# Optimization experiments

Measured on AMD Instinct MI355X. Metric: run time of the kernel, lower is better.

Reference implementation:

```python
import jax, jax.numpy as jnp
import numpy as np

MARGIN = 0.3


def setup_inputs() -> dict:
    key = jax.random.key(0)
    k1, k2 = jax.random.split(key)
    embeddings = jax.random.normal(k1, (4096, 128), dtype=jnp.float32)
    labels = jax.random.randint(k2, (4096,), 0, 256, dtype=jnp.int64)
    return {"embeddings": embeddings, "labels": labels}


def reference(embeddings, labels):
    # L2-normalize rows (same as F.normalize(p=2, dim=1), eps=1e-12)
    norm = jnp.maximum(jnp.linalg.norm(embeddings, axis=1, keepdims=True), 1e-12)
    e = embeddings / norm
    # cosine distance matrix [N, N]
    dist = 1.0 - e @ e.T

    same = labels[None, :] == labels[:, None]          # [N, N]
    n = labels.shape[0]
    eye = jnp.eye(n, dtype=bool)
    pos_mask = same & ~eye                             # positives excl. self
    neg_mask = ~same

    # dist in [0, 2]; finite sentinels keep max/min well-defined per row
    hardest_pos = jnp.max(jnp.where(pos_mask, dist, -1.0), axis=1)
    hardest_neg = jnp.min(jnp.where(neg_mask, dist, 3.0), axis=1)

    valid = jnp.any(pos_mask, axis=1) & jnp.any(neg_mask, axis=1)
    per_row = jax.nn.relu(hardest_pos - hardest_neg + MARGIN)
    loss_sum = jnp.sum(jnp.where(valid, per_row, 0.0))
    count = jnp.sum(valid)
    return loss_sum / jnp.maximum(count, 1).astype(loss_sum.dtype)
```

## Files before the change

### kernel.cpp

```cpp
#include <hip/hip_runtime.h>
#include <stdint.h>

typedef __bf16 bf16x8 __attribute__((ext_vector_type(8)));
typedef float f32x4 __attribute__((ext_vector_type(4)));

#define N_ROWS 4096
#define KD 128
#define BM 64
#define BN 64
#define NCHUNK 16
#define CHUNK 256
#define NBLOCKS (64 * NCHUNK)

__device__ __forceinline__ unsigned f2key(float f) {
    unsigned b = __float_as_uint(f);
    return (b & 0x80000000u) ? ~b : (b | 0x80000000u);
}
__device__ __forceinline__ float key2f(unsigned k) {
    unsigned b = (k & 0x80000000u) ? (k ^ 0x80000000u) : ~k;
    return __uint_as_float(b);
}

__device__ __forceinline__ unsigned short f32_to_bf16_rne(float f) {
    union { float f; uint32_t u; } v; v.f = f;
    uint32_t u = v.u;
    return (unsigned short)((u + 0x7FFFu + ((u >> 16) & 1u)) >> 16);
}

__global__ __launch_bounds__(256) void normalize_kernel(const float* __restrict__ E,
                                                        unsigned short* __restrict__ out,
                                                        unsigned* __restrict__ minkey,
                                                        unsigned* __restrict__ maxkey,
                                                        unsigned* __restrict__ ticket) {
    const int wave = threadIdx.x >> 6;
    const int lane = threadIdx.x & 63;
    const int row = blockIdx.x * 4 + wave;
    if (lane == 0) {
        minkey[row] = f2key(2.0f);
        maxkey[row] = f2key(-2.0f);
    }
    if (blockIdx.x == 0 && threadIdx.x == 0) *ticket = 0u;
    const float2 v = *(const float2*)&E[row * KD + lane * 2];
    float s = v.x * v.x + v.y * v.y;
#pragma unroll
    for (int m = 1; m < 64; m <<= 1) s += __shfl_xor(s, m, 64);
    float inv = 0.0f;
    if (s > 0.0f) {
        inv = rsqrtf(s);
        inv = inv * (1.5f - 0.5f * s * inv * inv);
    }
    const unsigned short a = f32_to_bf16_rne(v.x * inv);
    const unsigned short b = f32_to_bf16_rne(v.y * inv);
    ((uint32_t*)out)[row * (KD / 2) + lane] = ((uint32_t)b << 16) | a;
}

__global__ __launch_bounds__(256) void gram_kernel(const unsigned short* __restrict__ Ebits,
                                                   const int* __restrict__ labels,
                                                   unsigned* __restrict__ minkey,
                                                   unsigned* __restrict__ maxkey,
                                                   unsigned* __restrict__ ticket,
                                                   float* __restrict__ out) {
    __shared__ uint4 As4[BM * KD / 8];
    __shared__ uint4 Bs4[BN * KD / 8];
    __shared__ int ljs[CHUNK];
    __shared__ unsigned s_old;
    __shared__ float ssum[4];
    __shared__ int scnt[4];

    const int tid = threadIdx.x;
    const int itile = blockIdx.x & 63;
    const int chunk = blockIdx.x >> 6;
    const int ibase = itile * BM;
    const int cbase = chunk * CHUNK;

    {
        const uint4* src = (const uint4*)(Ebits + (size_t)ibase * KD);
#pragma unroll
        for (int it = 0; it < 4; ++it) {
            const int L = it * 256 + tid;
            const int t = L >> 8, s = (L >> 6) & 3, q = (L >> 4) & 3, l = L & 15;
            As4[L] = src[(t * 16 + l) * 16 + s * 4 + q];
        }
        ljs[tid] = labels[cbase + tid];
    }
    __syncthreads();

    const int wave = tid >> 6, lane = tid & 63;
    const int quad = lane >> 4, l15 = lane & 15;

    bf16x8 afrag[4];
#pragma unroll
    for (int s = 0; s < 4; ++s) afrag[s] = *(const bf16x8*)&As4[(wave * 4 + s) * 64 + lane];

    int li_lab[4];
#pragma unroll
    for (int r = 0; r < 4; ++r) li_lab[r] = labels[ibase + wave * 16 + quad * 4 + r];

    float minpos[4] = {2.0f, 2.0f, 2.0f, 2.0f};
    float maxneg[4] = {-2.0f, -2.0f, -2.0f, -2.0f};

    for (int jt = 0; jt < CHUNK / BN; ++jt) {
        const int jbase = cbase + jt * BN;
        __syncthreads();
        {
            const uint4* src = (const uint4*)(Ebits + (size_t)jbase * KD);
#pragma unroll
            for (int it = 0; it < 4; ++it) {
                const int L = it * 256 + tid;
                const int t = L >> 8, s = (L >> 6) & 3, q = (L >> 4) & 3, l = L & 15;
                Bs4[L] = src[(t * 16 + l) * 16 + s * 4 + q];
            }
        }
        __syncthreads();

#pragma unroll
        for (int t = 0; t < 4; ++t) {
            f32x4 acc = {0.f, 0.f, 0.f, 0.f};
#pragma unroll
            for (int s = 0; s < 4; ++s) {
                const bf16x8 bfrag = *(const bf16x8*)&Bs4[(t * 4 + s) * 64 + lane];
                acc = __builtin_amdgcn_mfma_f32_16x16x32_bf16(afrag[s], bfrag, acc, 0, 0, 0);
            }
            const int jg = jbase + t * 16 + l15;
            const int lj = ljs[jt * BN + t * 16 + l15];
#pragma unroll
            for (int r = 0; r < 4; ++r) {
                const int ig = ibase + wave * 16 + quad * 4 + r;
                const float d = acc[r];
                const bool same = (lj == li_lab[r]);
                const float dp = (same && (ig != jg)) ? d : 2.0f;
                const float dn = same ? -2.0f : d;
                minpos[r] = fminf(minpos[r], dp);
                maxneg[r] = fmaxf(maxneg[r], dn);
            }
        }
    }

#pragma unroll
    for (int m = 1; m < 16; m <<= 1) {
#pragma unroll
        for (int r = 0; r < 4; ++r) {
            minpos[r] = fminf(minpos[r], __shfl_xor(minpos[r], m, 64));
            maxneg[r] = fmaxf(maxneg[r], __shfl_xor(maxneg[r], m, 64));
        }
    }
    if (l15 == 0) {
#pragma unroll
        for (int r = 0; r < 4; ++r) {
            const int row = ibase + wave * 16 + quad * 4 + r;
            atomicMin(&minkey[row], f2key(minpos[r]));
            atomicMax(&maxkey[row], f2key(maxneg[r]));
        }
    }

    __syncthreads();
    if (tid == 0) s_old = atomicAdd(ticket, 1u);
    __syncthreads();
    if (s_old == (unsigned)(NBLOCKS - 1)) {
        float sum = 0.f;
        int cnt = 0;
        for (int row = tid; row < N_ROWS; row += 256) {
            const unsigned mpk = __hip_atomic_load(&minkey[row], __ATOMIC_RELAXED,
                                                   __HIP_MEMORY_SCOPE_AGENT);
            const unsigned mnk = __hip_atomic_load(&maxkey[row], __ATOMIC_RELAXED,
                                                   __HIP_MEMORY_SCOPE_AGENT);
            const float mp = key2f(mpk);
            const float mn = key2f(mnk);
            if (mp < 1.5f && mn > -1.5f) {
                sum += fmaxf(0.f, mn - mp + 0.3f);
                cnt += 1;
            }
        }
#pragma unroll
        for (int m = 1; m < 64; m <<= 1) {
            sum += __shfl_xor(sum, m, 64);
            cnt += __shfl_xor(cnt, m, 64);
        }
        if ((tid & 63) == 0) { ssum[tid >> 6] = sum; scnt[tid >> 6] = cnt; }
        __syncthreads();
        if (tid == 0) {
            const float S = ssum[0] + ssum[1] + ssum[2] + ssum[3];
            const int C = scnt[0] + scnt[1] + scnt[2] + scnt[3];
            out[0] = S / (float)(C > 0 ? C : 1);
        }
    }
}

extern "C" void kernel_launch(void* const* d_in, const int* in_sizes, int n_in,
                              void* d_out, int out_size, void* d_ws, size_t ws_size,
                              hipStream_t stream) {
    const float* E = (const float*)d_in[0];
    const int* labels = (const int*)d_in[1];

    unsigned short* ebits = (unsigned short*)d_ws;
    unsigned* minkey = (unsigned*)((char*)d_ws + (size_t)N_ROWS * KD * 2);
    unsigned* maxkey = minkey + N_ROWS;
    unsigned* ticket = maxkey + N_ROWS;
    float* out = (float*)d_out;

    normalize_kernel<<<N_ROWS / 4, 256, 0, stream>>>(E, ebits, minkey, maxkey, ticket);
    gram_kernel<<<NBLOCKS, 256, 0, stream>>>(ebits, labels, minkey, maxkey, ticket, out);
}
```

Before: 87.06 us.

## Prefetch B tiles into registers, swizzle LDS layout, rotate tile order

Global loads for the next B tile are issued into registers before the MFMA work on the current tile, then written to LDS between barriers, overlapping memory latency with compute. LDS now uses an XOR swizzle with coalesced global reads in place of the permuted gather. Tile order is rotated per i-tile to spread L2 traffic, and the diagonal check is skipped outside diagonal blocks. The final reduction is unrolled to batch atomic loads. This adds register pressure and still needs two barriers per tile.

After: 90.95 us. 1.04x slower.

```diff
diff --git a/kernel.cpp b/kernel.cpp
--- a/kernel.cpp
+++ b/kernel.cpp
@@ -10,6 +10,7 @@
 #define BN 64
 #define NCHUNK 16
 #define CHUNK 256
+#define JT (CHUNK / BN)
 #define NBLOCKS (64 * NCHUNK)
 
 __device__ __forceinline__ unsigned f2key(float f) {
@@ -26,6 +27,9 @@
     uint32_t u = v.u;
     return (unsigned short)((u + 0x7FFFu + ((u >> 16) & 1u)) >> 16);
 }
+
+__device__ __forceinline__ int swz(int row, int c) { return row * 16 + (c ^ (row & 15)); }
+__device__ __forceinline__ int swzL(int L) { return (L & ~15) | ((L & 15) ^ ((L >> 4) & 15)); }
 
 __global__ __launch_bounds__(256) void normalize_kernel(const float* __restrict__ E,
                                                         unsigned short* __restrict__ out,
@@ -72,68 +76,79 @@
     const int chunk = blockIdx.x >> 6;
     const int ibase = itile * BM;
     const int cbase = chunk * CHUNK;
-
+    const bool diagBlock = ((ibase >> 8) == chunk);
+
+    uint4 areg[4], breg[4];
     {
-        const uint4* src = (const uint4*)(Ebits + (size_t)ibase * KD);
-#pragma unroll
-        for (int it = 0; it < 4; ++it) {
-            const int L = it * 256 + tid;
-            const int t = L >> 8, s = (L >> 6) & 3, q = (L >> 4) & 3, l = L & 15;
-            As4[L] = src[(t * 16 + l) * 16 + s * 4 + q];
-        }
+        const uint4* asrc = (const uint4*)(Ebits + (size_t)ibase * KD);
+        const int rot0 = itile & (JT - 1);
+        const uint4* bsrc = (const uint4*)(Ebits + (size_t)(cbase + rot0 * BN) * KD);
+#pragma unroll
+        for (int it = 0; it < 4; ++it) areg[it] = asrc[it * 256 + tid];
+#pragma unroll
+        for (int it = 0; it < 4; ++it) breg[it] = bsrc[it * 256 + tid];
         ljs[tid] = labels[cbase + tid];
+#pragma unroll
+        for (int it = 0; it < 4; ++it) As4[swzL(it * 256 + tid)] = areg[it];
+#pragma unroll
+        for (int it = 0; it < 4; ++it) Bs4[swzL(it * 256 + tid)] = breg[it];
     }
     __syncthreads();
 
     const int wave = tid >> 6, lane = tid & 63;
     const int quad = lane >> 4, l15 = lane & 15;
+    const int igb = ibase + wave * 16 + quad * 4;
 
     bf16x8 afrag[4];
 #pragma unroll
-    for (int s = 0; s < 4; ++s) afrag[s] = *(const bf16x8*)&As4[(wave * 4 + s) * 64 + lane];
+    for (int s = 0; s < 4; ++s) afrag[s] = *(const bf16x8*)&As4[swz(wave * 16 + l15, s * 4 + quad)];
 
     int li_lab[4];
 #pragma unroll
-    for (int r = 0; r < 4; ++r) li_lab[r] = labels[ibase + wave * 16 + quad * 4 + r];
+    for (int r = 0; r < 4; ++r) li_lab[r] = labels[igb + r];
 
     float minpos[4] = {2.0f, 2.0f, 2.0f, 2.0f};
     float maxneg[4] = {-2.0f, -2.0f, -2.0f, -2.0f};
 
-    for (int jt = 0; jt < CHUNK / BN; ++jt) {
-        const int jbase = cbase + jt * BN;
-        __syncthreads();
-        {
-            const uint4* src = (const uint4*)(Ebits + (size_t)jbase * KD);
-#pragma unroll
-            for (int it = 0; it < 4; ++it) {
-                const int L = it * 256 + tid;
-                const int t = L >> 8, s = (L >> 6) & 3, q = (L >> 4) & 3, l = L & 15;
-                Bs4[L] = src[(t * 16 + l) * 16 + s * 4 + q];
-            }
-        }
-        __syncthreads();
+    for (int p = 0; p < JT; ++p) {
+        const int rot = (p + itile) & (JT - 1);
+        const int jbase = cbase + rot * BN;
+
+        if (p + 1 < JT) {
+            const int rotn = (p + 1 + itile) & (JT - 1);
+            const uint4* bsrc = (const uint4*)(Ebits + (size_t)(cbase + rotn * BN) * KD);
+#pragma unroll
+            for (int it = 0; it < 4; ++it) breg[it] = bsrc[it * 256 + tid];
+        }
 
 #pragma unroll
         for (int t = 0; t < 4; ++t) {
             f32x4 acc = {0.f, 0.f, 0.f, 0.f};
 #pragma unroll
             for (int s = 0; s < 4; ++s) {
-                const bf16x8 bfrag = *(const bf16x8*)&Bs4[(t * 4 + s) * 64 + lane];
+                const bf16x8 bfrag = *(const bf16x8*)&Bs4[swz(t * 16 + l15, s * 4 + quad)];
                 acc = __builtin_amdgcn_mfma_f32_16x16x32_bf16(afrag[s], bfrag, acc, 0, 0, 0);
             }
             const int jg = jbase + t * 16 + l15;
-            const int lj = ljs[jt * BN + t * 16 + l15];
+            const int lj = ljs[rot * BN + t * 16 + l15];
 #pragma unroll
             for (int r = 0; r < 4; ++r) {
-                const int ig = ibase + wave * 16 + quad * 4 + r;
                 const float d = acc[r];
                 const bool same = (lj == li_lab[r]);
-                const float dp = (same && (ig != jg)) ? d : 2.0f;
+                const bool excl = diagBlock && (igb + r == jg);
+                const float dp = (same && !excl) ? d : 2.0f;
                 const float dn = same ? -2.0f : d;
                 minpos[r] = fminf(minpos[r], dp);
                 maxneg[r] = fmaxf(maxneg[r], dn);
             }
         }
+
+        if (p + 1 < JT) {
+            __syncthreads();
+#pragma unroll
+            for (int it = 0; it < 4; ++it) Bs4[swzL(it * 256 + tid)] = breg[it];
+            __syncthreads();
+        }
     }
 
 #pragma unroll
@@ -147,9 +162,8 @@
     if (l15 == 0) {
 #pragma unroll
         for (int r = 0; r < 4; ++r) {
-            const int row = ibase + wave * 16 + quad * 4 + r;
-            atomicMin(&minkey[row], f2key(minpos[r]));
-            atomicMax(&maxkey[row], f2key(maxneg[r]));
+            atomicMin(&minkey[igb + r], f2key(minpos[r]));
+            atomicMax(&maxkey[igb + r], f2key(maxneg[r]));
         }
     }
 
@@ -159,16 +173,25 @@
     if (s_old == (unsigned)(NBLOCKS - 1)) {
         float sum = 0.f;
         int cnt = 0;
-        for (int row = tid; row < N_ROWS; row += 256) {
-            const unsigned mpk = __hip_atomic_load(&minkey[row], __ATOMIC_RELAXED,
-                                                   __HIP_MEMORY_SCOPE_AGENT);
-            const unsigned mnk = __hip_atomic_load(&maxkey[row], __ATOMIC_RELAXED,
-                                                   __HIP_MEMORY_SCOPE_AGENT);
-            const float mp = key2f(mpk);
-            const float mn = key2f(mnk);
-            if (mp < 1.5f && mn > -1.5f) {
-                sum += fmaxf(0.f, mn - mp + 0.3f);
-                cnt += 1;
+        unsigned mpk[8], mnk[8];
+#pragma unroll
+        for (int half = 0; half < 2; ++half) {
+#pragma unroll
+            for (int u = 0; u < 8; ++u) {
+                const int row = tid + 256 * (half * 8 + u);
+                mpk[u] = __hip_atomic_load(&minkey[row], __ATOMIC_RELAXED,
+                                           __HIP_MEMORY_SCOPE_AGENT);
+                mnk[u] = __hip_atomic_load(&maxkey[row], __ATOMIC_RELAXED,
+                                           __HIP_MEMORY_SCOPE_AGENT);
+            }
+#pragma unroll
+            for (int u = 0; u < 8; ++u) {
+                const float mp = key2f(mpk[u]);
+                const float mn = key2f(mnk[u]);
+                if (mp < 1.5f && mn > -1.5f) {
+                    sum += fmaxf(0.f, mn - mp + 0.3f);
+                    cnt += 1;
+                }
             }
         }
 #pragma unroll
```
